# Kernel optimization log

Measured on AMD Instinct MI355X. Metric: run time of the kernel, lower is better.

Reference implementation:

```python
import jax, jax.numpy as jnp
import numpy as np

N_NODES = 50000
N_GRAPHS = 250
NODES_PER_GRAPH = 200
EDGES_PER_GRAPH = 3200  # avg degree 16
F_IN = 128
EMB = 128
HID = 128
VOCAB = 1000
N_REL = 8


def setup_inputs() -> dict:
    key = jax.random.key(0)
    ks = jax.random.split(key, 16)

    # message: col 0 = discrete token id (stored as float), col 1 = continuous value
    disc = jax.random.randint(ks[0], (N_GRAPHS,), 0, VOCAB).astype(jnp.float32)
    cont = jax.random.normal(ks[1], (N_GRAPHS,), dtype=jnp.float32)
    message = jnp.stack([disc, cont], axis=1)  # [B, 2]

    x = jax.random.normal(ks[2], (N_NODES, F_IN), dtype=jnp.float32)

    # within-graph edges: local indices + per-graph node offset
    offs = (jnp.arange(N_GRAPHS, dtype=jnp.int64) * NODES_PER_GRAPH)[:, None]
    src = (jax.random.randint(ks[3], (N_GRAPHS, EDGES_PER_GRAPH), 0, NODES_PER_GRAPH) + offs).reshape(-1)
    dst = (jax.random.randint(ks[4], (N_GRAPHS, EDGES_PER_GRAPH), 0, NODES_PER_GRAPH) + offs).reshape(-1)
    edge_index = jnp.stack([src, dst], axis=0).astype(jnp.int64)  # [2, E]
    edge_type = jax.random.randint(ks[5], (N_GRAPHS * EDGES_PER_GRAPH,), 0, N_REL).astype(jnp.int64)

    batch = jnp.repeat(jnp.arange(N_GRAPHS, dtype=jnp.int64), NODES_PER_GRAPH)  # [N]

    s = 0.05
    W1 = jax.random.normal(ks[6], (N_REL, F_IN, EMB), dtype=jnp.float32) * s
    root1 = jax.random.normal(ks[7], (F_IN, EMB), dtype=jnp.float32) * s
    b1 = jnp.zeros((EMB,), dtype=jnp.float32)
    W2 = jax.random.normal(ks[8], (N_REL, EMB, EMB), dtype=jnp.float32) * s
    root2 = jax.random.normal(ks[9], (EMB, EMB), dtype=jnp.float32) * s
    b2 = jnp.zeros((EMB,), dtype=jnp.float32)
    embed_table = jax.random.normal(ks[10], (VOCAB, EMB), dtype=jnp.float32) * s
    cont_w = jax.random.normal(ks[11], (1, EMB), dtype=jnp.float32) * s
    cont_b = jnp.zeros((EMB,), dtype=jnp.float32)
    msg_w = jax.random.normal(ks[12], (2 * EMB, HID), dtype=jnp.float32) * s
    msg_b = jnp.zeros((HID,), dtype=jnp.float32)

    return {
        "message": message, "x": x, "edge_index": edge_index, "edge_type": edge_type,
        "batch": batch, "max_nodes": NODES_PER_GRAPH,
        "W1": W1, "root1": root1, "b1": b1, "W2": W2, "root2": root2, "b2": b2,
        "embed_table": embed_table, "cont_w": cont_w, "cont_b": cont_b,
        "msg_w": msg_w, "msg_b": msg_b,
    }


def _rgcn_conv(h, src, dst, edge_type, W, root, b, n_nodes, n_rel):
    # per-node per-relation transform, then gather per edge: avoids [E,F,F] weight gather
    hW = jnp.einsum('nf,rfo->nro', h, W)          # [N, R, O]
    msg = hW[src, edge_type]                       # [E, O]
    # mean aggregation per (dst, relation) as in PyG RGCNConv(aggr='mean')
    key_dr = dst * n_rel + edge_type
    cnt = jax.ops.segment_sum(jnp.ones_like(edge_type, dtype=h.dtype), key_dr,
                              num_segments=n_nodes * n_rel)
    norm = 1.0 / jnp.maximum(cnt[key_dr], 1.0)     # [E]
    agg = jax.ops.segment_sum(msg * norm[:, None], dst, num_segments=n_nodes)  # [N, O]
    return agg + h @ root + b


def reference(message, x, edge_index, edge_type, batch, max_nodes,
              W1, root1, b1, W2, root2, b2,
              embed_table, cont_w, cont_b, msg_w, msg_b):
    n_nodes = x.shape[0]
    n_rel = W1.shape[0]
    n_graphs = message.shape[0]
    src, dst = edge_index[0], edge_index[1]

    # --- RGCN node embeddings (2 layers, ReLU between) ---
    h = _rgcn_conv(x, src, dst, edge_type, W1, root1, b1, n_nodes, n_rel)
    h = jax.nn.relu(h)
    node_emb = _rgcn_conv(h, src, dst, edge_type, W2, root2, b2, n_nodes, n_rel)  # [N, EMB]

    # --- message representation ---
    disc_tok = message[:, 0].astype(jnp.int32)
    disc_emb = embed_table[disc_tok]                                   # [B, EMB]
    cont_emb = jax.nn.relu(message[:, 1:2] @ cont_w + cont_b)          # [B, EMB]
    combined = jnp.concatenate([disc_emb, cont_emb], axis=1)           # [B, 2*EMB]
    message_repr = jax.nn.relu(combined @ msg_w + msg_b)               # [B, HID]

    # --- per-node dot score against its graph's message, padded per graph ---
    scores = jnp.einsum('ne,ne->n', node_emb, message_repr[batch])     # [N]
    counts = jax.ops.segment_sum(jnp.ones((n_nodes,), dtype=jnp.int32), batch,
                                 num_segments=n_graphs)
    start = jnp.cumsum(counts) - counts                                # exclusive cumsum
    pos = jnp.arange(n_nodes) - start[batch]                           # slot within graph
    logits = jnp.full((n_graphs, max_nodes), -jnp.inf, dtype=scores.dtype)
    logits = logits.at[batch, pos].set(scores)
    return logits
```

## Files before the change

### kernel.cpp

```cpp
#include <hip/hip_runtime.h>
#include <stdint.h>

#define G_   250
#define P_   200
#define EPG  3200
#define E_   800000
#define F_   128
#define R_   8
#define HROW 136
#define NKEY (R_ * P_)

typedef _Float16 f16x8 __attribute__((ext_vector_type(8)));
typedef _Float16 f16x4 __attribute__((ext_vector_type(4)));
typedef float    f32x4 __attribute__((ext_vector_type(4)));
typedef float    f32x16 __attribute__((ext_vector_type(16)));

__global__ __launch_bounds__(256) void k_wstage(const float* __restrict__ W1, const float* __restrict__ root1,
                                                const float* __restrict__ W2, const float* __restrict__ root2,
                                                _Float16* __restrict__ wf) {
  int t = blockIdx.x * 256 + threadIdx.x;
  if (t >= 2 * 9 * 8 * 4 * 64 * 8) return;
  int j = t & 7;
  int rest = t >> 3;
  int lane = rest & 63; rest >>= 6;
  int ntj = rest & 3;   rest >>= 2;
  int kt = rest & 7;    rest >>= 3;
  int r = rest % 9;
  int l = rest / 9;
  int k = kt * 16 + (lane >> 5) * 8 + j;
  int n = ntj * 32 + (lane & 31);
  const float* Wl = (l == 0) ? W1 : W2;
  const float* rl = (l == 0) ? root1 : root2;
  float v = (r < 8) ? Wl[(r * F_ + k) * F_ + n] : rl[k * F_ + n];
  wf[t] = (_Float16)v;
}

__global__ __launch_bounds__(512, 2) void k_main(
    const float* __restrict__ x, const int* __restrict__ ei, const int* __restrict__ et,
    const _Float16* __restrict__ wf, const float* __restrict__ b1, const float* __restrict__ b2,
    const float* __restrict__ message, const float* __restrict__ embed,
    const float* __restrict__ cw, const float* __restrict__ cb,
    const float* __restrict__ mw, const float* __restrict__ mb,
    float* __restrict__ out) {
  __shared__ __attribute__((aligned(16))) _Float16 hbuf0[P_ * HROW];
  __shared__ __attribute__((aligned(16))) _Float16 hbuf1[P_ * HROW];
  __shared__ unsigned short csrS[EPG];
  __shared__ int offsS[NKEY + 1];
  __shared__ float msgS[F_ + 1];

  int g = blockIdx.x, tid = threadIdx.x;
  int lane = tid & 63, wave = tid >> 6;
  int m32 = lane & 31, kh = lane >> 5;

  int*   Sint     = (int*)hbuf1;
  int*   cnt      = Sint;
  int*   cur      = Sint + 1600;
  int*   chunkTot = Sint + 3200;
  int*   scanA    = Sint + 3400;
  int*   scanB    = Sint + 3656;
  float* comb     = (float*)(Sint + 3912);
  float* red      = comb + 256;
  int*   eRec     = (int*)(red + 512);

  for (int i = tid; i < P_ * 32; i += 512) {
    int row = i >> 5, c4 = i & 31;
    const float4 v = ((const float4*)x)[(g * P_ + row) * 32 + c4];
    f16x4 pk = { (_Float16)v.x, (_Float16)v.y, (_Float16)v.z, (_Float16)v.w };
    *((f16x4*)&hbuf0[row * HROW + c4 * 4]) = pk;
  }
  for (int i = tid; i < NKEY; i += 512) { cnt[i] = 0; cur[i] = 0; }
  if (tid < F_) {
    int tok = (int)message[g * 2];
    float cont = message[g * 2 + 1];
    comb[tid] = embed[tok * F_ + tid];
    float ce = cont * cw[tid] + cb[tid];
    comb[F_ + tid] = ce > 0.0f ? ce : 0.0f;
  }
  __syncthreads();
  int base = g * EPG, nbase = g * P_;
  for (int e = tid; e < EPG; e += 512) {
    int s = ei[base + e] - nbase;
    int d = ei[E_ + base + e] - nbase;
    int r = et[base + e];
    eRec[e] = s | (d << 8) | (r << 16);
    atomicAdd(&cnt[r * P_ + d], 1);
  }
  __syncthreads();
  if (tid < 200) {
    int s = 0;
    for (int i = 0; i < 8; i++) { int c = cnt[tid * 8 + i]; offsS[tid * 8 + i] = s; s += c; }
    chunkTot[tid] = s;
    scanA[tid] = s;
  }
  __syncthreads();
  {
    int* src = scanA; int* dst = scanB;
    for (int st = 1; st < 256; st <<= 1) {
      if (tid < 200) dst[tid] = src[tid] + (tid >= st ? src[tid - st] : 0);
      __syncthreads();
      int* tmp = src; src = dst; dst = tmp;
    }
  }
  if (tid < 200) {
    int add = scanA[tid] - chunkTot[tid];
    for (int i = 0; i < 8; i++) offsS[tid * 8 + i] += add;
  }
  if (tid == 0) offsS[NKEY] = EPG;
  {
    int col = tid & 127, seg = tid >> 7;
    float acc = 0.0f;
#pragma unroll 8
    for (int k = seg * 64; k < seg * 64 + 64; k++) acc += comb[k] * mw[k * F_ + col];
    red[tid] = acc;
  }
  __syncthreads();
  for (int e = tid; e < EPG; e += 512) {
    int rec = eRec[e];
    int s = rec & 255, d = (rec >> 8) & 255, r = rec >> 16;
    int key = r * P_ + d;
    int pos = atomicAdd(&cur[key], 1);
    csrS[offsS[key] + pos] = (unsigned short)s;
  }
  if (tid < F_) {
    float a = mb[tid] + red[tid] + red[128 + tid] + red[256 + tid] + red[384 + tid];
    a = a > 0.0f ? a : 0.0f;
    msgS[tid] = a;
    comb[tid] = a * b2[tid];
  }
  __syncthreads();
  if (tid < 64) comb[tid] += comb[tid + 64];
  __syncthreads();
  if (tid < 32) comb[tid] += comb[tid + 32];
  __syncthreads();
  if (tid < 16) comb[tid] += comb[tid + 16];
  __syncthreads();
  if (tid == 0) {
    float s = 0.0f;
    for (int i = 0; i < 16; i++) s += comb[i];
    msgS[F_] = s;
  }
  __syncthreads();

  int jobBase = wave * 25;
  bool rowAct = (m32 < 25);
  int myD = jobBase + m32;
  int ck = kh * 8;

  for (int l = 0; l < 2; l++) {
    const _Float16* Ap = (l == 0) ? hbuf0 : hbuf1;
    f32x16 acc[4];
#pragma unroll
    for (int nt = 0; nt < 4; nt++)
#pragma unroll
      for (int i = 0; i < 16; i++) acc[nt][i] = 0.0f;
    const _Float16* wl = wf + l * (9 * 8 * 4 * 64 * 8);
    for (int r = 0; r < 9; r++) {
      f16x8 Bf[8][4];
      const _Float16* wr = wl + r * (8 * 4 * 64 * 8);
#pragma unroll
      for (int kt = 0; kt < 8; kt++)
#pragma unroll
        for (int nt = 0; nt < 4; nt++)
          Bf[kt][nt] = *((const f16x8*)(wr + ((kt * 4 + nt) * 64 + lane) * 8));
      f16x8 a[8];
      if (r < 8) {
        int o = 0, n = 0;
        if (rowAct) { int key = r * P_ + myD; o = offsS[key]; n = offsS[key + 1] - o; }
        f16x8 z = {0, 0, 0, 0, 0, 0, 0, 0};
#pragma unroll
        for (int kt = 0; kt < 8; kt++) a[kt] = z;
        int sNext = (n > 0) ? (int)csrS[o] : 0;
        for (int t = 0; t < n; t++) {
          int sc = sNext;
          if (t + 1 < n) sNext = (int)csrS[o + t + 1];
          const _Float16* hp = &Ap[sc * HROW + ck];
#pragma unroll
          for (int kt = 0; kt < 8; kt++) a[kt] += *((const f16x8*)(hp + kt * 16));
        }
        float nf = (n > 0) ? 1.0f / (float)n : 0.0f;
        _Float16 nh = (_Float16)nf;
#pragma unroll
        for (int kt = 0; kt < 8; kt++) a[kt] *= nh;
      } else {
        int rowA = jobBase + (rowAct ? m32 : 24);
        const _Float16* hp = &Ap[rowA * HROW + ck];
#pragma unroll
        for (int kt = 0; kt < 8; kt++) a[kt] = *((const f16x8*)(hp + kt * 16));
      }
#pragma unroll
      for (int kt = 0; kt < 8; kt++)
#pragma unroll
        for (int nt = 0; nt < 4; nt++)
          acc[nt] = __builtin_amdgcn_mfma_f32_32x32x16_f16(a[kt], Bf[kt][nt], acc[nt], 0, 0, 0);
    }
    if (l == 0) {
#pragma unroll
      for (int nt = 0; nt < 4; nt++) {
        int col = nt * 32 + m32;
        float bias = b1[col];
#pragma unroll
        for (int reg = 0; reg < 16; reg++) {
          int row = (reg & 3) + 8 * (reg >> 2) + 4 * kh;
          if (row < 25) {
            float v = acc[nt][reg] + bias;
            v = v > 0.0f ? v : 0.0f;
            hbuf1[(jobBase + row) * HROW + col] = (_Float16)v;
          }
        }
      }
      __syncthreads();
    } else {
      float db2 = msgS[F_];
#pragma unroll
      for (int reg = 0; reg < 16; reg++) {
        int row = (reg & 3) + 8 * (reg >> 2) + 4 * kh;
        float p = 0.0f;
#pragma unroll
        for (int nt = 0; nt < 4; nt++)
          p += acc[nt][reg] * msgS[nt * 32 + m32];
        p += __shfl_xor(p, 16, 32);
        p += __shfl_xor(p, 8, 32);
        p += __shfl_xor(p, 4, 32);
        p += __shfl_xor(p, 2, 32);
        p += __shfl_xor(p, 1, 32);
        if (m32 == 0 && row < 25)
          out[g * P_ + jobBase + row] = p + db2;
      }
    }
  }
}

extern "C" void kernel_launch(void* const* d_in, const int* in_sizes, int n_in,
                              void* d_out, int out_size, void* d_ws, size_t ws_size,
                              hipStream_t stream) {
  const float* message = (const float*)d_in[0];
  const float* x       = (const float*)d_in[1];
  const int*   ei      = (const int*)d_in[2];
  const int*   et      = (const int*)d_in[3];
  const float* W1      = (const float*)d_in[6];
  const float* root1   = (const float*)d_in[7];
  const float* b1      = (const float*)d_in[8];
  const float* W2      = (const float*)d_in[9];
  const float* root2   = (const float*)d_in[10];
  const float* b2      = (const float*)d_in[11];
  const float* embed   = (const float*)d_in[12];
  const float* cw      = (const float*)d_in[13];
  const float* cb      = (const float*)d_in[14];
  const float* mw      = (const float*)d_in[15];
  const float* mb      = (const float*)d_in[16];

  _Float16* wfrag = (_Float16*)d_ws;
  float*    out   = (float*)d_out;

  hipLaunchKernelGGL(k_wstage, dim3(1152), dim3(256), 0, stream, W1, root1, W2, root2, wfrag);
  hipLaunchKernelGGL(k_main, dim3(G_), dim3(512), 0, stream, x, ei, et, wfrag, b1, b2,
                     message, embed, cw, cb, mw, mb, out);
}
```

Before: 189.7 us.

## Restructure preprocessing with warp scan, split waves, and stream B fragments per column tile

The weight staging kernel now reads the source matrices coalesced and scatters into the fragment layout. Preprocessing splits waves so edge counting overlaps the message MLP, and the multi-barrier block scan becomes a single-wave shuffle scan. The main MFMA loop loads B fragments one column tile at a time with double buffering instead of holding all 32 fragments, which cuts register pressure. A barrier is added before layer 0 writes into hbuf1, because that buffer is also used as scratch for the CSR data.

```diff
diff --git a/kernel.cpp b/kernel.cpp
--- a/kernel.cpp
+++ b/kernel.cpp
@@ -19,20 +19,16 @@
                                                 const float* __restrict__ W2, const float* __restrict__ root2,
                                                 _Float16* __restrict__ wf) {
   int t = blockIdx.x * 256 + threadIdx.x;
-  if (t >= 2 * 9 * 8 * 4 * 64 * 8) return;
-  int j = t & 7;
-  int rest = t >> 3;
-  int lane = rest & 63; rest >>= 6;
-  int ntj = rest & 3;   rest >>= 2;
-  int kt = rest & 7;    rest >>= 3;
-  int r = rest % 9;
-  int l = rest / 9;
-  int k = kt * 16 + (lane >> 5) * 8 + j;
-  int n = ntj * 32 + (lane & 31);
+  int n = t & 127;
+  int k = (t >> 7) & 127;
+  int rl_ = t >> 14;
+  int r = rl_ % 9, l = rl_ / 9;
   const float* Wl = (l == 0) ? W1 : W2;
-  const float* rl = (l == 0) ? root1 : root2;
-  float v = (r < 8) ? Wl[(r * F_ + k) * F_ + n] : rl[k * F_ + n];
-  wf[t] = (_Float16)v;
+  const float* rt = (l == 0) ? root1 : root2;
+  float v = (r < 8) ? Wl[(r * F_ + k) * F_ + n] : rt[k * F_ + n];
+  int lane = (n & 31) | (((k >> 3) & 1) << 5);
+  int j = k & 7, kt = k >> 4, ntj = n >> 5;
+  wf[((((l * 9 + r) * 8 + kt) * 4 + ntj) * 64 + lane) * 8 + j] = (_Float16)v;
 }
 
 __global__ __launch_bounds__(512, 2) void k_main(
@@ -52,15 +48,12 @@
   int lane = tid & 63, wave = tid >> 6;
   int m32 = lane & 31, kh = lane >> 5;
 
-  int*   Sint     = (int*)hbuf1;
-  int*   cnt      = Sint;
-  int*   cur      = Sint + 1600;
-  int*   chunkTot = Sint + 3200;
-  int*   scanA    = Sint + 3400;
-  int*   scanB    = Sint + 3656;
-  float* comb     = (float*)(Sint + 3912);
-  float* red      = comb + 256;
-  int*   eRec     = (int*)(red + 512);
+  int*   Sint = (int*)hbuf1;
+  int*   cnt  = Sint;
+  int*   cur  = Sint + 1600;
+  int*   eRec = Sint + 3200;
+  float* comb = (float*)(Sint + 6400);
+  float* red  = (float*)(Sint + 6656);
 
   for (int i = tid; i < P_ * 32; i += 512) {
     int row = i >> 5, c4 = i & 31;
@@ -77,43 +70,63 @@
     comb[F_ + tid] = ce > 0.0f ? ce : 0.0f;
   }
   __syncthreads();
+
   int base = g * EPG, nbase = g * P_;
-  for (int e = tid; e < EPG; e += 512) {
-    int s = ei[base + e] - nbase;
-    int d = ei[E_ + base + e] - nbase;
-    int r = et[base + e];
-    eRec[e] = s | (d << 8) | (r << 16);
-    atomicAdd(&cnt[r * P_ + d], 1);
-  }
-  __syncthreads();
-  if (tid < 200) {
-    int s = 0;
-    for (int i = 0; i < 8; i++) { int c = cnt[tid * 8 + i]; offsS[tid * 8 + i] = s; s += c; }
-    chunkTot[tid] = s;
-    scanA[tid] = s;
-  }
-  __syncthreads();
-  {
-    int* src = scanA; int* dst = scanB;
-    for (int st = 1; st < 256; st <<= 1) {
-      if (tid < 200) dst[tid] = src[tid] + (tid >= st ? src[tid - st] : 0);
-      __syncthreads();
-      int* tmp = src; src = dst; dst = tmp;
-    }
-  }
-  if (tid < 200) {
-    int add = scanA[tid] - chunkTot[tid];
-    for (int i = 0; i < 8; i++) offsS[tid * 8 + i] += add;
-  }
-  if (tid == 0) offsS[NKEY] = EPG;
-  {
-    int col = tid & 127, seg = tid >> 7;
+  if (wave < 6) {
+    for (int e = wave * 64 + lane; e < EPG; e += 384) {
+      int s = ei[base + e] - nbase;
+      int d = ei[E_ + base + e] - nbase;
+      int r = et[base + e];
+      eRec[e] = s | (d << 8) | (r << 16);
+      atomicAdd(&cnt[r * P_ + d], 1);
+    }
+  } else {
+    int col = tid & 127;
     float acc = 0.0f;
-#pragma unroll 8
-    for (int k = seg * 64; k < seg * 64 + 64; k++) acc += comb[k] * mw[k * F_ + col];
-    red[tid] = acc;
-  }
-  __syncthreads();
+#pragma unroll 16
+    for (int k2 = 0; k2 < 256; k2++) acc += comb[k2] * mw[k2 * F_ + col];
+    red[col] = acc;
+  }
+  __syncthreads();
+
+  if (wave == 0) {
+    int4 vv[8];
+    int osum = 0;
+    if (lane < 50) {
+      const int4* cp = (const int4*)(cnt + lane * 32);
+#pragma unroll
+      for (int i = 0; i < 8; i++) { vv[i] = cp[i]; osum += vv[i].x + vv[i].y + vv[i].z + vv[i].w; }
+    }
+    int incl = osum;
+#pragma unroll
+    for (int d = 1; d < 64; d <<= 1) {
+      int t2 = __shfl_up(incl, d, 64);
+      if (lane >= d) incl += t2;
+    }
+    int run = incl - osum;
+    if (lane < 50) {
+#pragma unroll
+      for (int i = 0; i < 8; i++) {
+        offsS[lane * 32 + i * 4 + 0] = run; run += vv[i].x;
+        offsS[lane * 32 + i * 4 + 1] = run; run += vv[i].y;
+        offsS[lane * 32 + i * 4 + 2] = run; run += vv[i].z;
+        offsS[lane * 32 + i * 4 + 3] = run; run += vv[i].w;
+      }
+    }
+    if (lane == 0) offsS[NKEY] = EPG;
+  } else if (wave == 1) {
+    float m0 = mb[lane] + red[lane];
+    float m1 = mb[lane + 64] + red[lane + 64];
+    m0 = m0 > 0.0f ? m0 : 0.0f;
+    m1 = m1 > 0.0f ? m1 : 0.0f;
+    msgS[lane] = m0; msgS[lane + 64] = m1;
+    float p = m0 * b2[lane] + m1 * b2[lane + 64];
+#pragma unroll
+    for (int d = 32; d > 0; d >>= 1) p += __shfl_xor(p, d, 64);
+    if (lane == 0) msgS[F_] = p;
+  }
+  __syncthreads();
+
   for (int e = tid; e < EPG; e += 512) {
     int rec = eRec[e];
     int s = rec & 255, d = (rec >> 8) & 255, r = rec >> 16;
@@ -121,24 +134,6 @@
     int pos = atomicAdd(&cur[key], 1);
     csrS[offsS[key] + pos] = (unsigned short)s;
   }
-  if (tid < F_) {
-    float a = mb[tid] + red[tid] + red[128 + tid] + red[256 + tid] + red[384 + tid];
-    a = a > 0.0f ? a : 0.0f;
-    msgS[tid] = a;
-    comb[tid] = a * b2[tid];
-  }
-  __syncthreads();
-  if (tid < 64) comb[tid] += comb[tid + 64];
-  __syncthreads();
-  if (tid < 32) comb[tid] += comb[tid + 32];
-  __syncthreads();
-  if (tid < 16) comb[tid] += comb[tid + 16];
-  __syncthreads();
-  if (tid == 0) {
-    float s = 0.0f;
-    for (int i = 0; i < 16; i++) s += comb[i];
-    msgS[F_] = s;
-  }
   __syncthreads();
 
   int jobBase = wave * 25;
@@ -155,13 +150,11 @@
       for (int i = 0; i < 16; i++) acc[nt][i] = 0.0f;
     const _Float16* wl = wf + l * (9 * 8 * 4 * 64 * 8);
     for (int r = 0; r < 9; r++) {
-      f16x8 Bf[8][4];
       const _Float16* wr = wl + r * (8 * 4 * 64 * 8);
+      f16x8 Bn[8];
 #pragma unroll
       for (int kt = 0; kt < 8; kt++)
-#pragma unroll
-        for (int nt = 0; nt < 4; nt++)
-          Bf[kt][nt] = *((const f16x8*)(wr + ((kt * 4 + nt) * 64 + lane) * 8));
+        Bn[kt] = *((const f16x8*)(wr + ((kt * 4 + 0) * 64 + lane) * 8));
       f16x8 a[8];
       if (r < 8) {
         int o = 0, n = 0;
@@ -188,12 +181,24 @@
         for (int kt = 0; kt < 8; kt++) a[kt] = *((const f16x8*)(hp + kt * 16));
       }
 #pragma unroll
-      for (int kt = 0; kt < 8; kt++)
-#pragma unroll
-        for (int nt = 0; nt < 4; nt++)
-          acc[nt] = __builtin_amdgcn_mfma_f32_32x32x16_f16(a[kt], Bf[kt][nt], acc[nt], 0, 0, 0);
+      for (int nt = 0; nt < 4; nt++) {
+        f16x8 Bx[8];
+        if (nt < 3) {
+#pragma unroll
+          for (int kt = 0; kt < 8; kt++)
+            Bx[kt] = *((const f16x8*)(wr + ((kt * 4 + nt + 1) * 64 + lane) * 8));
+        }
+#pragma unroll
+        for (int kt = 0; kt < 8; kt++)
+          acc[nt] = __builtin_amdgcn_mfma_f32_32x32x16_f16(a[kt], Bn[kt], acc[nt], 0, 0, 0);
+        if (nt < 3) {
+#pragma unroll
+          for (int kt = 0; kt < 8; kt++) Bn[kt] = Bx[kt];
+        }
+      }
     }
     if (l == 0) {
+      __syncthreads();
 #pragma unroll
       for (int nt = 0; nt < 4; nt++) {
         int col = nt * 32 + m32;
```

New measurement: 195.7 us. 1.03x slower.
